# Performance work log

Measured on AMD Instinct MI355X. Metric: run time of the kernel, lower is better.

The kernel has to match this reference:

```python
import jax, jax.numpy as jnp
import numpy as np

NUM_HEADS = 16
LN_EPS = 1e-5


def pos_encoding(length, d):
    pos = jnp.arange(length, dtype=jnp.float32)[:, None]
    i = jnp.arange(d, dtype=jnp.float32)[None, :]
    angle = pos / jnp.power(10000.0, (2.0 * jnp.floor(i / 2.0)) / d)
    return jnp.where((jnp.arange(d) % 2) == 0, jnp.sin(angle), jnp.cos(angle))


def rel_shift(x):
    # x: (B, H, l, m) -> TXL shift trick
    b, h, l, m = x.shape
    x = jnp.concatenate([x, jnp.zeros((b, h, l, 1), x.dtype)], axis=-1)
    x = x.reshape(b, h, l * (m + 1))
    return x[:, :, l - 1:-1].reshape(b, h, l, m)


def layer_norm(x, g, b):
    mu = jnp.mean(x, axis=-1, keepdims=True)
    var = jnp.mean(jnp.square(x - mu), axis=-1, keepdims=True)
    return (x - mu) * jax.lax.rsqrt(var + LN_EPS) * g + b


def setup_inputs() -> dict:
    key = jax.random.key(0)
    B, S, M, D, L, V = 2, 1024, 1024, 1024, 4, 32000
    ks = jax.random.split(key, 32)
    s = 0.02
    d = {
        'inputs': jax.random.randint(ks[0], (B, S), 0, V, dtype=jnp.int32),
        'mems': jax.random.normal(ks[1], (L, B, M, D), jnp.float32),
        'emb': jax.random.normal(ks[2], (V, D), jnp.float32) * s,
        'Wq': jax.random.normal(ks[3], (L, D, D), jnp.float32) * s,
        'bq': jnp.zeros((L, D), jnp.float32),
        'Wke': jax.random.normal(ks[4], (L, D, D), jnp.float32) * s,
        'bke': jnp.zeros((L, D), jnp.float32),
        'Wkr': jax.random.normal(ks[5], (L, D, D), jnp.float32) * s,
        'bkr': jnp.zeros((L, D), jnp.float32),
        'Wv': jax.random.normal(ks[6], (L, D, D), jnp.float32) * s,
        'bv': jnp.zeros((L, D), jnp.float32),
        'Wo': jax.random.normal(ks[7], (L, D, D), jnp.float32) * s,
        'bo': jnp.zeros((L, D), jnp.float32),
        'ln1_g': jnp.ones((L, D), jnp.float32),
        'ln1_b': jnp.zeros((L, D), jnp.float32),
        'W1': jax.random.normal(ks[8], (L, D, D), jnp.float32) * s,
        'b1': jnp.zeros((L, D), jnp.float32),
        'W2': jax.random.normal(ks[9], (L, D, D), jnp.float32) * s,
        'b2': jnp.zeros((L, D), jnp.float32),
        'ln2_g': jnp.ones((L, D), jnp.float32),
        'ln2_b': jnp.zeros((L, D), jnp.float32),
        'Wh': jax.random.normal(ks[10], (D, D), jnp.float32) * s,
        'bh': jnp.zeros((D,), jnp.float32),
        'Wf': jax.random.normal(ks[11], (D, V), jnp.float32) * s,
        'bf': jnp.zeros((V,), jnp.float32),
        'next_mem_len': 1024,
    }
    return d


def reference(inputs, mems, emb, Wq, bq, Wke, bke, Wkr, bkr, Wv, bv, Wo, bo,
              ln1_g, ln1_b, W1, b1, W2, b2, ln2_g, ln2_b, Wh, bh, Wf, bf,
              next_mem_len):
    B, S = inputs.shape
    L, _, M, D = mems.shape
    T = M + S
    H = NUM_HEADS
    dh = D // H
    sqrt_dk = jnp.sqrt(jnp.float32(dh))

    rel_enc = pos_encoding(T, D)[::-1]  # (T, D), reversed
    # look-ahead mask: query i may attend key j iff j <= i + M
    mask = (jnp.arange(T)[None, :] > (jnp.arange(S)[:, None] + M)).astype(jnp.float32)
    mask = mask[None, None] * -1e9  # (1,1,S,T)

    x = emb[inputs] * jnp.sqrt(jnp.float32(D))  # (B,S,D)

    for l in range(L):
        x_tilde = jnp.concatenate([mems[l], x], axis=1)  # (B,T,D)
        q = (x @ Wq[l] + bq[l]).reshape(B, S, H, dh).transpose(0, 2, 1, 3)
        k = (x_tilde @ Wke[l] + bke[l]).reshape(B, T, H, dh).transpose(0, 2, 1, 3)
        v = (x_tilde @ Wv[l] + bv[l]).reshape(B, T, H, dh).transpose(0, 2, 1, 3)
        A = jnp.einsum('bhsd,bhtd->bhst', q, k)
        Qr = (rel_enc @ Wkr[l] + bkr[l]).reshape(T, H, dh).transpose(1, 0, 2)  # (H,T,dh)
        B_hat = jnp.einsum('bhsd,htd->bhst', q, Qr)
        score = (A + rel_shift(B_hat)) / sqrt_dk + mask
        attn = jax.nn.softmax(score, axis=-1)
        ctx = jnp.einsum('bhst,bhtd->bhsd', attn, v)
        ctx = ctx.transpose(0, 2, 1, 3).reshape(B, S, D)
        attn_out = ctx @ Wo[l] + bo[l]
        h1 = layer_norm(x + attn_out, ln1_g[l], ln1_b[l])
        ff = jax.nn.gelu(h1 @ W1[l] + b1[l], approximate=False) @ W2[l] + b2[l]
        x = layer_norm(h1 + ff, ln2_g[l], ln2_b[l])

    x = jax.nn.gelu(x @ Wh + bh, approximate=False)
    logits = x @ Wf + bf
    return logits
```

## Files before the change

### kernel.cpp

```cpp
#include <hip/hip_runtime.h>
#include <hip/hip_bf16.h>
#include <math.h>

typedef __attribute__((ext_vector_type(4))) float f32x4;
typedef __attribute__((ext_vector_type(8))) short s16x8;

#define BB 2
#define SS 1024
#define MEM 1024
#define DD 1024
#define LL 4
#define VV 32000
#define TT 2048
#define NH 16
#define DH 64

__device__ __forceinline__ short f2bf(float f) {
    unsigned u = __float_as_uint(f);
    u += 0x7fffu + ((u >> 16) & 1u);
    return (short)(u >> 16);
}

__device__ __forceinline__ float gelu_f(float x) {
    return 0.5f * x * (1.0f + erff(x * 0.70710678118654752f));
}

__device__ __forceinline__ void gll16(const short* g, short* l) {
    __builtin_amdgcn_global_load_lds(
        (__attribute__((address_space(1))) void*)(short*)g,
        (__attribute__((address_space(3))) void*)l, 16, 0, 0);
}

template<int WM, int WN>
__global__ __launch_bounds__(256) void gemm_k128(
    const short* __restrict__ A, const short* __restrict__ Bt,
    const float* __restrict__ bias, const float* __restrict__ bias2,
    int nsplit, void* __restrict__ Cv, int N, int K, int nby, int act, int obf)
{
    constexpr int BM = WM * 32, BN = WN * 32;
    constexpr int NA = BM / 16, NB = BN / 16;
    __shared__ short a_s[BM * 128];
    __shared__ short b_s[BN * 128];
    const int tid  = threadIdx.x;
    const int lane = tid & 63;
    const int wave = tid >> 6;
    const int wr = wave >> 1, wc = wave & 1;
    const int fr = lane & 15, fg = lane >> 4;

    const int nwg = gridDim.x;
    const int bid = blockIdx.x;
    const int swz = ((nwg & 7) == 0) ? ((bid & 7) * (nwg >> 3) + (bid >> 3)) : bid;
    const size_t m0 = (size_t)(swz % nby) * BM;
    const size_t n0 = (size_t)(swz / nby) * BN;

    const short* gA[NA]; short* lA[NA];
    const short* gB[NB]; short* lB[NB];
    #pragma unroll
    for (int i = 0; i < NA; ++i) {
        gA[i] = A + (m0 + i * 16 + (tid & 15)) * (size_t)K + (tid >> 4) * 8;
        lA[i] = &a_s[(i * 256 + tid) * 8];
    }
    #pragma unroll
    for (int i = 0; i < NB; ++i) {
        gB[i] = Bt + (n0 + i * 16 + (tid & 15)) * (size_t)K + (tid >> 4) * 8;
        lB[i] = &b_s[(i * 256 + tid) * 8];
    }

    f32x4 acc[WM][WN] = {};

    #pragma unroll
    for (int i = 0; i < NA; ++i) gll16(gA[i], lA[i]);
    #pragma unroll
    for (int i = 0; i < NB; ++i) gll16(gB[i], lB[i]);

    const int nt = K >> 7;
    for (int t = 0; t < nt; ++t) {
        __syncthreads();
        s16x8 af[WM][4], bf[WN][4];
        #pragma unroll
        for (int mi = 0; mi < WM; ++mi)
            #pragma unroll
            for (int h = 0; h < 4; ++h)
                af[mi][h] = *(const s16x8*)&a_s[((wr*WM + mi)*256 + (4*h + fg)*16 + fr) * 8];
        #pragma unroll
        for (int ni = 0; ni < WN; ++ni)
            #pragma unroll
            for (int h = 0; h < 4; ++h)
                bf[ni][h] = *(const s16x8*)&b_s[((wc*WN + ni)*256 + (4*h + fg)*16 + fr) * 8];
        if (t + 1 < nt) {
            __syncthreads();
            const int koff = (t + 1) << 7;
            #pragma unroll
            for (int i = 0; i < NA; ++i) gll16(gA[i] + koff, lA[i]);
            #pragma unroll
            for (int i = 0; i < NB; ++i) gll16(gB[i] + koff, lB[i]);
        }
        #pragma unroll
        for (int mi = 0; mi < WM; ++mi)
            #pragma unroll
            for (int ni = 0; ni < WN; ++ni)
                #pragma unroll
                for (int h = 0; h < 4; ++h)
                    acc[mi][ni] = __builtin_amdgcn_mfma_f32_16x16x32_bf16(
                        af[mi][h], bf[ni][h], acc[mi][ni], 0, 0, 0);
    }

    float* Cf = (float*)Cv;
    short* Cb = (short*)Cv;
    #pragma unroll
    for (int mi = 0; mi < WM; ++mi) {
        #pragma unroll
        for (int ni = 0; ni < WN; ++ni) {
            const size_t r0 = m0 + wr*WM*16 + mi*16 + fg*4;
            const size_t c  = n0 + wc*WN*16 + ni*16 + fr;
            const float bb = (c < (size_t)nsplit) ? bias[c] : bias2[c - nsplit];
            #pragma unroll
            for (int rg = 0; rg < 4; ++rg) {
                float vv = acc[mi][ni][rg] + bb;
                if (act) vv = gelu_f(vv);
                if (obf) Cb[(r0 + rg)*(size_t)N + c] = f2bf(vv);
                else     Cf[(r0 + rg)*(size_t)N + c] = vv;
            }
        }
    }
}

#define READ_A8(MH, BUF) \
  _Pragma("unroll") for (int mf = 0; mf < 4; ++mf) \
  _Pragma("unroll") for (int kh = 0; kh < 2; ++kh) \
    aA[mf][kh] = *(const s16x8*)&lds[(BUF)*16384 + WR*8192 + (((MH)*4+mf)*128 + (kh*4+fg)*16 + fr)*8];

#define READ_B8(BUF) \
  _Pragma("unroll") for (int nf = 0; nf < 4; ++nf) \
  _Pragma("unroll") for (int kh = 0; kh < 2; ++kh) \
    bB[nf][kh] = *(const s16x8*)&lds[32768 + (BUF)*16384 + BH*8192 + ((BC4+nf)*128 + (kh*4+fg)*16 + fr)*8];

#define QUAD8(MH, NHX) \
  _Pragma("unroll") for (int mf = 0; mf < 4; ++mf) \
  _Pragma("unroll") for (int n2 = 0; n2 < 2; ++n2) { \
    acc[(MH)*4+mf][(NHX)*2+n2] = __builtin_amdgcn_mfma_f32_16x16x32_bf16( \
        aA[mf][0], bB[(NHX)*2+n2][0], acc[(MH)*4+mf][(NHX)*2+n2], 0, 0, 0); \
    acc[(MH)*4+mf][(NHX)*2+n2] = __builtin_amdgcn_mfma_f32_16x16x32_bf16( \
        aA[mf][1], bB[(NHX)*2+n2][1], acc[(MH)*4+mf][(NHX)*2+n2], 0, 0, 0); }

#define STAGE_A8(HH, BUF, KT) { \
    const short* g = pA0 + (HH)*(128*1024) + (KT)*64; \
    short* l = &lds[(BUF)*16384 + (HH)*8192 + tid*8]; \
    gll16(g, l); gll16(g + 64*1024, l + 512*8); }

#define STAGE_B8(HH, BUF, KT) { \
    const short* g = pB0 + (HH)*(128*1024) + (KT)*64; \
    short* l = &lds[32768 + (BUF)*16384 + (HH)*8192 + tid*8]; \
    gll16(g, l); gll16(g + 64*1024, l + 512*8); }

#define PHASE8(BUF, MH, NHX, RA, RB, SMAT, SH, SBUF, SKT, VMW) { \
    if (RA) { READ_A8(MH, BUF) } \
    if (RB) { READ_B8(BUF) } \
    if ((SMAT) == 0) STAGE_A8(SH, SBUF, SKT) else STAGE_B8(SH, SBUF, SKT) \
    __builtin_amdgcn_s_barrier(); \
    asm volatile("s_waitcnt lgkmcnt(0)" ::: "memory"); \
    __builtin_amdgcn_sched_barrier(0); \
    __builtin_amdgcn_s_setprio(1); \
    QUAD8(MH, NHX) \
    __builtin_amdgcn_s_setprio(0); \
    if (VMW) { asm volatile("s_waitcnt vmcnt(4)" ::: "memory"); } \
    __builtin_amdgcn_s_barrier(); }

__global__ __launch_bounds__(512, 2) void gemm8p(
    const short* __restrict__ A, const short* __restrict__ Bt,
    const float* __restrict__ bias, float* __restrict__ C, int N)
{
    extern __shared__ short lds[];
    const int tid  = threadIdx.x;
    const int lane = tid & 63;
    const int wave = tid >> 6;
    const int WR = wave >> 2;
    const int WC = wave & 3;
    const int BH = WC >> 1;
    const int BC4 = (WC & 1) * 4;
    const int fr = lane & 15, fg = lane >> 4;

    const int nwg = gridDim.x;
    const int bid = blockIdx.x;
    const int swz = ((nwg & 7) == 0) ? ((bid & 7) * (nwg >> 3) + (bid >> 3)) : bid;
    const size_t m0 = (size_t)(swz % 8) * 256;
    const size_t n0 = (size_t)(swz / 8) * 256;

    const int arow0 = (tid >> 7) * 16 + (tid & 15);
    const int aks0  = ((tid >> 4) & 7) * 8;
    const short* pA0 = A  + (m0 + arow0) * 1024 + aks0;
    const short* pB0 = Bt + (n0 + arow0) * 1024 + aks0;

    f32x4 acc[8][4] = {};
    s16x8 aA[4][2], bB[4][2];

    STAGE_B8(0, 0, 0) STAGE_B8(1, 0, 0)
    STAGE_A8(0, 0, 0) STAGE_A8(1, 0, 0)
    STAGE_B8(0, 1, 1) STAGE_B8(1, 1, 1)
    asm volatile("s_waitcnt vmcnt(4)" ::: "memory");
    __builtin_amdgcn_s_barrier();

    for (int it = 0; it < 8; ++it) {
        const int k1 = 2*it + 1;
        int k2 = 2*it + 2; if (k2 > 15) k2 = 15;
        int k3 = 2*it + 3; if (k3 > 15) k3 = 15;
        PHASE8(0, 0, 0, 1, 1, 0, 0, 1, k1, 0)
        PHASE8(0, 0, 1, 0, 0, 0, 1, 1, k1, 0)
        PHASE8(0, 1, 0, 1, 0, 1, 0, 0, k2, 0)
        PHASE8(0, 1, 1, 0, 0, 1, 1, 0, k2, 1)
        PHASE8(1, 0, 0, 1, 1, 0, 0, 0, k2, 0)
        PHASE8(1, 0, 1, 0, 0, 0, 1, 0, k2, 0)
        PHASE8(1, 1, 0, 1, 0, 1, 0, 1, k3, 0)
        PHASE8(1, 1, 1, 0, 0, 1, 1, 1, k3, 1)
    }

    #pragma unroll
    for (int mf = 0; mf < 8; ++mf) {
        #pragma unroll
        for (int nf = 0; nf < 4; ++nf) {
            const size_t r0 = m0 + WR*128 + mf*16 + fg*4;
            const size_t c  = n0 + WC*64 + nf*16 + fr;
            const float bb = bias[c];
            #pragma unroll
            for (int rg = 0; rg < 4; ++rg)
                C[(r0 + rg) * (size_t)N + c] = acc[mf][nf][rg] + bb;
        }
    }
}

__global__ __launch_bounds__(512, 2) void gemm8n(
    const short* __restrict__ A, const short* __restrict__ Bt,
    const float* __restrict__ bA, const float* __restrict__ bBp,
    const float* __restrict__ bCp, int s1, int s2,
    short* __restrict__ Cb, int N, int K, int nby)
{
    extern __shared__ short lds[];
    const int tid  = threadIdx.x;
    const int lane = tid & 63;
    const int wave = tid >> 6;
    const int WR = wave >> 2;
    const int WC = wave & 3;
    const int fr = lane & 15, fg = lane >> 4;

    const int nwg = gridDim.x;
    const int bid = blockIdx.x;
    const int swz = ((nwg & 7) == 0) ? ((bid & 7) * (nwg >> 3) + (bid >> 3)) : bid;
    const size_t m0 = (size_t)(swz % nby) * 256;
    const size_t n0 = (size_t)(swz / nby) * 128;

    const int rA  = (tid >> 7) * 16 + (tid & 15);
    const int ks8 = ((tid >> 4) & 7) * 8;
    const short* pA = A  + (m0 + rA) * (size_t)K + ks8;
    const short* pB = Bt + (n0 + rA) * (size_t)K + ks8;

    auto stageA = [&](int kt, int h, int buf) {
        const short* g = pA + (size_t)(h * 128) * K + kt * 64;
        short* l = &lds[buf * 16384 + h * 8192 + tid * 8];
        gll16(g, l);
        gll16(g + (size_t)64 * K, l + 512 * 8);
    };
    auto stageB = [&](int kt, int buf) {
        const short* g = pB + kt * 64;
        short* l = &lds[49152 + buf * 8192 + tid * 8];
        gll16(g, l);
        gll16(g + (size_t)64 * K, l + 512 * 8);
    };

    f32x4 acc[8][2] = {};
    const int nt = K >> 6;

    stageB(0, 0); stageA(0, 0, 0); stageA(0, 1, 0);
    stageA(1, 0, 1); stageA(1, 1, 1); stageB(1, 1);

    for (int J = 0; J < nt / 2; ++J) {
        const int t0 = 2 * J, t1 = 2 * J + 1;
        const int b0 = t0 % 3, b1 = t1 % 3;
        const int b2 = (t0 + 2) % 3, b3 = (t1 + 2) % 3;
        int s2k = t0 + 2; if (s2k >= nt) s2k = nt - 1;
        int s3k = t1 + 2; if (s3k >= nt) s3k = nt - 1;

        #pragma unroll
        for (int ph = 0; ph < 2; ++ph) {
            const int bt = ph ? b1 : b0;
            asm volatile("s_waitcnt vmcnt(6)" ::: "memory");
            __builtin_amdgcn_s_barrier();
            __builtin_amdgcn_sched_barrier(0);
            if (ph == 0) { stageB(s2k, b2); stageA(s2k, 0, b2); stageA(s2k, 1, b2); }
            else         { stageA(s3k, 0, b3); stageA(s3k, 1, b3); stageB(s3k, b3); }
            s16x8 bB[2][2];
            #pragma unroll
            for (int nf = 0; nf < 2; ++nf)
                #pragma unroll
                for (int kh = 0; kh < 2; ++kh)
                    bB[nf][kh] = *(const s16x8*)&lds[49152 + bt*8192 +
                        ((WC*2 + nf)*128 + (kh*4 + fg)*16 + fr) * 8];
            #pragma unroll
            for (int MH = 0; MH < 2; ++MH) {
                s16x8 aF[4][2];
                #pragma unroll
                for (int mf = 0; mf < 4; ++mf)
                    #pragma unroll
                    for (int kh = 0; kh < 2; ++kh)
                        aF[mf][kh] = *(const s16x8*)&lds[bt*16384 + WR*8192 +
                            ((MH*4 + mf)*128 + (kh*4 + fg)*16 + fr) * 8];
                asm volatile("s_waitcnt lgkmcnt(0)" ::: "memory");
                __builtin_amdgcn_sched_barrier(0);
                __builtin_amdgcn_s_setprio(1);
                #pragma unroll
                for (int mf = 0; mf < 4; ++mf)
                    #pragma unroll
                    for (int nf = 0; nf < 2; ++nf) {
                        acc[MH*4+mf][nf] = __builtin_amdgcn_mfma_f32_16x16x32_bf16(
                            aF[mf][0], bB[nf][0], acc[MH*4+mf][nf], 0, 0, 0);
                        acc[MH*4+mf][nf] = __builtin_amdgcn_mfma_f32_16x16x32_bf16(
                            aF[mf][1], bB[nf][1], acc[MH*4+mf][nf], 0, 0, 0);
                    }
                __builtin_amdgcn_s_setprio(0);
            }
        }
    }

    #pragma unroll
    for (int mf = 0; mf < 8; ++mf) {
        #pragma unroll
        for (int nf = 0; nf < 2; ++nf) {
            const size_t r0 = m0 + WR*128 + mf*16 + fg*4;
            const size_t c  = n0 + WC*32 + nf*16 + fr;
            const float bb = (c < (size_t)s1) ? bA[c]
                            : (c < (size_t)s2) ? bBp[c - s1] : bCp[c - s2];
            #pragma unroll
            for (int rg = 0; rg < 4; ++rg)
                Cb[(r0 + rg) * (size_t)N + c] = f2bf(acc[mf][nf][rg] + bb);
        }
    }
}

__global__ __launch_bounds__(256) void transpose7_kernel(
    const float* w0, const float* w1, const float* w2, const float* w3,
    const float* w4, const float* w5, const float* w6, short* out)
{
    __shared__ float t[32][33];
    const int z = blockIdx.z;
    const float* W;
    switch (z) {
        case 0: W = w0; break; case 1: W = w1; break; case 2: W = w2; break;
        case 3: W = w3; break; case 4: W = w4; break; case 5: W = w5; break;
        default: W = w6; break;
    }
    short* O = out + (size_t)z * DD * DD;
    const int tid = threadIdx.x;
    const int k0 = blockIdx.y * 32, n0 = blockIdx.x * 32;
    const int r = tid >> 3, c4 = (tid & 7) * 4;
    float4 v = *(const float4*)&W[(size_t)(k0 + r) * DD + n0 + c4];
    t[r][c4+0] = v.x; t[r][c4+1] = v.y; t[r][c4+2] = v.z; t[r][c4+3] = v.w;
    __syncthreads();
    short4 o;
    o.x = f2bf(t[c4+0][r]); o.y = f2bf(t[c4+1][r]);
    o.z = f2bf(t[c4+2][r]); o.w = f2bf(t[c4+3][r]);
    *(short4*)&O[(size_t)(n0 + r) * DD + k0 + c4] = o;
}

__global__ __launch_bounds__(256) void transposeF_kernel(
    const float* __restrict__ W, short* __restrict__ O)
{
    __shared__ float t[32][33];
    const int tid = threadIdx.x;
    const int k0 = blockIdx.y * 32, n0 = blockIdx.x * 32;
    const int r = tid >> 3, c4 = (tid & 7) * 4;
    float4 v = *(const float4*)&W[(size_t)(k0 + r) * VV + n0 + c4];
    t[r][c4+0] = v.x; t[r][c4+1] = v.y; t[r][c4+2] = v.z; t[r][c4+3] = v.w;
    __syncthreads();
    short4 o;
    o.x = f2bf(t[c4+0][r]); o.y = f2bf(t[c4+1][r]);
    o.z = f2bf(t[c4+2][r]); o.w = f2bf(t[c4+3][r]);
    *(short4*)&O[(size_t)(n0 + r) * DD + k0 + c4] = o;
}

__global__ __launch_bounds__(256, 2) void attn_kernel(
    const short* __restrict__ q, const short* __restrict__ k,
    const short* __restrict__ v, const short* __restrict__ Qr,
    short* __restrict__ ctx, int kstr, int qstr)
{
    __shared__ short k_s[128][72];
    __shared__ short vT_s[64][136];
    __shared__ short qr_s[192][72];
    __shared__ float a_t[64][68];

    const int tid  = threadIdx.x;
    const int id   = blockIdx.x;
    const int bh   = id & 31;
    const int qi   = ((id >> 5) + bh) & 15;
    const int q0   = qi * 64;
    const int b    = bh >> 4;
    const int h    = bh & 15;
    const int hoff = h * DH;

    const int lane = tid & 63;
    const int wave = tid >> 6;
    const int fr   = lane & 15;
    const int fg   = lane >> 4;
    const int tk2 = tid >> 1, ck2 = (tid & 1) * 32;
    const int jq2 = tid >> 1, dqr = (tid & 1) * 32;
    const int j2  = tid >> 2, dq2 = (tid & 3) * 16;
    const int sr  = tid >> 2;
    const int sc0 = (tid & 3) * 16;

    const short* qrow = q + ((size_t)(b * TT + q0 + 16 * wave + fr)) * kstr + hoff;
    s16x8 aq0 = *(const s16x8*)(qrow + fg * 8);
    s16x8 aq1 = *(const s16x8*)(qrow + 32 + fg * 8);

    float m_r = -1e30f, l_r = 0.0f;

    const int t_end = q0 + 64 + MEM;
    const int u0b   = SS - 1 - q0 - 63;

    s16x8 kf[4], vf[4], rgq[4], rgq2[2];
    auto loadKV = [&](int t0n) {
        const short* kp = k + ((size_t)(b * TT + t0n + tk2)) * kstr + hoff + ck2;
        const short* vp = v + ((size_t)(b * TT + t0n + tk2)) * kstr + hoff + ck2;
        #pragma unroll
        for (int i = 0; i < 4; ++i) {
            kf[i] = *(const s16x8*)(kp + 8 * i);
            vf[i] = *(const s16x8*)(vp + 8 * i);
        }
    };
    auto loadQR = [&](int t0n) {
        int u = t0n + u0b + 63 + jq2;
        u = u > TT - 1 ? TT - 1 : u;
        const short* rp = Qr + (size_t)u * qstr + hoff + dqr;
        #pragma unroll
        for (int i = 0; i < 4; ++i) rgq[i] = *(const s16x8*)(rp + 8 * i);
    };
    {
        int u1 = u0b + jq2;
        u1 = u1 > TT - 1 ? TT - 1 : u1;
        const short* rp1 = Qr + (size_t)u1 * qstr + hoff + dqr;
        #pragma unroll
        for (int i = 0; i < 4; ++i) rgq[i] = *(const s16x8*)(rp1 + 8 * i);
        int u2 = u0b + 128 + j2;
        u2 = u2 > TT - 1 ? TT - 1 : u2;
        const short* rp2 = Qr + (size_t)u2 * qstr + hoff + dq2;
        rgq2[0] = *(const s16x8*)rp2;
        rgq2[1] = *(const s16x8*)(rp2 + 8);
    }
    loadKV(0);

    f32x4 opv[4] = {};
    const int nlo = 3 - wave, nhi = 7 - wave;
    int rb = 0;

    auto computeHalf = [&](int hh, int t0) {
        {
            __builtin_amdgcn_s_setprio(1);
            #pragma unroll
            for (int n = 0; n < 4; ++n) {
                s16x8 b0 = *(const s16x8*)&k_s[64*hh + 16*n + fr][fg * 8];
                s16x8 b1 = *(const s16x8*)&k_s[64*hh + 16*n + fr][32 + fg * 8];
                f32x4 ca = {0, 0, 0, 0};
                ca = __builtin_amdgcn_mfma_f32_16x16x32_bf16(aq0, b0, ca, 0, 0, 0);
                ca = __builtin_amdgcn_mfma_f32_16x16x32_bf16(aq1, b1, ca, 0, 0, 0);
                #pragma unroll
                for (int rg = 0; rg < 4; ++rg)
                    a_t[16*wave + 4*fg + rg][16*n + fr] = ca[rg];
            }
            __builtin_amdgcn_s_setprio(0);
        }
        {
            #pragma unroll
            for (int n = 0; n < 8; ++n) {
                if (n < nlo || n > nhi) continue;
                int pr = rb + 64*hh + 16*n + fr;
                if (pr >= 192) pr -= 192;
                s16x8 c0 = *(const s16x8*)&qr_s[pr][fg * 8];
                s16x8 c1 = *(const s16x8*)&qr_s[pr][32 + fg * 8];
                f32x4 cb = {0, 0, 0, 0};
                cb = __builtin_amdgcn_mfma_f32_16x16x32_bf16(aq0, c0, cb, 0, 0, 0);
                cb = __builtin_amdgcn_mfma_f32_16x16x32_bf16(aq1, c1, cb, 0, 0, 0);
                #pragma unroll
                for (int rg = 0; rg < 4; ++rg) {
                    const int r  = 16*wave + 4*fg + rg;
                    const int tl = 16*n + fr - 63 + r;
                    if ((unsigned)tl < 64u) a_t[r][tl] += cb[rg];
                }
            }
        }
        {
            const int sg = q0 + sr;
            const int tb = t0 + 64*hh;
            float e[16];
            float mx = -1e30f;
            #pragma unroll
            for (int j = 0; j < 16; ++j) {
                const int c = sc0 + j;
                float x = a_t[sr][c] * 0.125f;
                x = (tb + c > sg + MEM) ? -1e30f : x;
                e[j] = x;
                mx = fmaxf(mx, x);
            }
            mx = fmaxf(mx, __shfl_xor(mx, 1, 64));
            mx = fmaxf(mx, __shfl_xor(mx, 2, 64));
            const float mn  = fmaxf(m_r, mx);
            const float scl = __expf(m_r - mn);
            float sum = 0.0f;
            s16x8 p0, p1;
            #pragma unroll
            for (int j = 0; j < 16; ++j) {
                float ev = __expf(e[j] - mn);
                sum += ev;
                if (j < 8) p0[j] = f2bf(ev); else p1[j - 8] = f2bf(ev);
            }
            sum += __shfl_xor(sum, 1, 64);
            sum += __shfl_xor(sum, 2, 64);
            l_r = l_r * scl + sum;
            m_r = mn;
            short* prow = (short*)&a_t[sr][0];
            *(s16x8*)&prow[sc0]     = p0;
            *(s16x8*)&prow[sc0 + 8] = p1;
            asm volatile("s_waitcnt lgkmcnt(0)" ::: "memory");
            __builtin_amdgcn_sched_barrier(0);

            f32x4 scv;
            #pragma unroll
            for (int rg = 0; rg < 4; ++rg) scv[rg] = __shfl(scl, 16*fg + 4*rg, 64);
            #pragma unroll
            for (int n = 0; n < 4; ++n)
                #pragma unroll
                for (int rg = 0; rg < 4; ++rg) opv[n][rg] *= scv[rg];
            const short* pv = (const short*)&a_t[16*wave + fr][0];
            s16x8 ap0 = *(const s16x8*)&pv[fg * 8];
            s16x8 ap1 = *(const s16x8*)&pv[32 + fg * 8];
            __builtin_amdgcn_s_setprio(1);
            #pragma unroll
            for (int n = 0; n < 4; ++n) {
                const int d  = 16*n + fr;
                const int xw = (d >> 3) & 3;
                s16x8 bv0 = *(const s16x8*)&vT_s[d][64*hh + (fg ^ xw) * 8];
                s16x8 bv1 = *(const s16x8*)&vT_s[d][64*hh + 32 + ((fg + 4) ^ xw ? 0 : 0) + (fg ^ xw) * 8 - (fg ^ xw) * 8 + ((fg ^ xw) * 8)];
                bv1 = *(const s16x8*)&vT_s[d][64*hh + 32 + (fg ^ xw) * 8];
                opv[n] = __builtin_amdgcn_mfma_f32_16x16x32_bf16(ap0, bv0, opv[n], 0, 0, 0);
                opv[n] = __builtin_amdgcn_mfma_f32_16x16x32_bf16(ap1, bv1, opv[n], 0, 0, 0);
            }
            __builtin_amdgcn_s_setprio(0);
        }
    };

    for (int t0 = 0; t0 < t_end; t0 += 128) {
        asm volatile("" ::: "memory");
        __builtin_amdgcn_s_barrier();
        __builtin_amdgcn_sched_barrier(0);
        {
            #pragma unroll
            for (int i = 0; i < 4; ++i)
                *(s16x8*)&k_s[tk2][ck2 + 8*i] = kf[i];
            #pragma unroll
            for (int i = 0; i < 4; ++i) {
                #pragma unroll
                for (int e = 0; e < 8; ++e) {
                    const int d = ck2 + 8*i + e;
                    const int col = 64*(tk2 >> 6) + ((tk2 & 63) ^ (((d >> 3) & 3) << 3));
                    vT_s[d][col] = vf[i][e];
                }
            }
            if (t0 == 0) {
                #pragma unroll
                for (int i = 0; i < 4; ++i)
                    *(s16x8*)&qr_s[jq2][dqr + 8*i] = rgq[i];
                *(s16x8*)&qr_s[128 + j2][dq2]     = rgq2[0];
                *(s16x8*)&qr_s[128 + j2][dq2 + 8] = rgq2[1];
            } else {
                int p = rb + 63 + jq2;
                if (p >= 192) p -= 192;
                #pragma unroll
                for (int i = 0; i < 4; ++i)
                    *(s16x8*)&qr_s[p][dqr + 8*i] = rgq[i];
            }
        }
        if (t0 + 128 < t_end) { loadKV(t0 + 128); loadQR(t0 + 128); }
        asm volatile("s_waitcnt lgkmcnt(0)" ::: "memory");
        __builtin_amdgcn_s_barrier();
        __builtin_amdgcn_sched_barrier(0);

        computeHalf(0, t0);
        if (t0 + 64 < t_end) computeHalf(1, t0);

        rb += 128; if (rb >= 192) rb -= 192;
    }

    {
        f32x4 lv;
        #pragma unroll
        for (int rg = 0; rg < 4; ++rg) lv[rg] = __shfl(l_r, 16*fg + 4*rg, 64);
        #pragma unroll
        for (int rg = 0; rg < 4; ++rg) {
            const int r = 16*wave + 4*fg + rg;
            const float inv = 1.0f / lv[rg];
            short* op = ctx + ((size_t)(b * SS + q0 + r)) * DD + hoff;
            #pragma unroll
            for (int n = 0; n < 4; ++n)
                op[16*n + fr] = f2bf(opv[n][rg] * inv);
        }
    }
}

__global__ __launch_bounds__(256) void addln_kernel(
    const float* __restrict__ a, const float* __restrict__ b,
    const float* __restrict__ g, const float* __restrict__ be,
    float* __restrict__ out32, short* __restrict__ outbf)
{
    __shared__ float red[8];
    const int row = blockIdx.x;
    const int tid = threadIdx.x;
    const size_t base = (size_t)row * DD;
    const int c = tid * 4;
    float4 xa = *(const float4*)(a + base + c);
    float4 xb = *(const float4*)(b + base + c);
    float x0 = xa.x + xb.x, x1 = xa.y + xb.y, x2 = xa.z + xb.z, x3 = xa.w + xb.w;
    float s  = x0 + x1 + x2 + x3;
    float sq = x0 * x0 + x1 * x1 + x2 * x2 + x3 * x3;
    #pragma unroll
    for (int o = 32; o > 0; o >>= 1) {
        s  += __shfl_down(s, o, 64);
        sq += __shfl_down(sq, o, 64);
    }
    const int wv = tid >> 6;
    if ((tid & 63) == 0) { red[wv * 2] = s; red[wv * 2 + 1] = sq; }
    __syncthreads();
    float ts = red[0] + red[2] + red[4] + red[6];
    float tq = red[1] + red[3] + red[5] + red[7];
    float mu  = ts * (1.0f / DD);
    float var = tq * (1.0f / DD) - mu * mu;
    float rs  = rsqrtf(var + 1e-5f);
    float4 gv = *(const float4*)(g + c);
    float4 bv = *(const float4*)(be + c);
    float4 o4;
    o4.x = (x0 - mu) * rs * gv.x + bv.x;
    o4.y = (x1 - mu) * rs * gv.y + bv.y;
    o4.z = (x2 - mu) * rs * gv.z + bv.z;
    o4.w = (x3 - mu) * rs * gv.w + bv.w;
    *(float4*)(out32 + base + c) = o4;
    short4 ob;
    ob.x = f2bf(o4.x); ob.y = f2bf(o4.y); ob.z = f2bf(o4.z); ob.w = f2bf(o4.w);
    *(short4*)(outbf + base + c) = ob;
}

__global__ __launch_bounds__(256) void embed_kernel(
    const int* __restrict__ inp, const float* __restrict__ emb,
    float* __restrict__ x32, short* __restrict__ xbf)
{
    const int row = blockIdx.x;
    const int c = threadIdx.x * 4;
    const int idx = inp[row];
    float4 vv = *(const float4*)(emb + (size_t)idx * DD + c);
    vv.x *= 32.0f; vv.y *= 32.0f; vv.z *= 32.0f; vv.w *= 32.0f;
    *(float4*)(x32 + (size_t)row * DD + c) = vv;
    short4 ob;
    ob.x = f2bf(vv.x); ob.y = f2bf(vv.y); ob.z = f2bf(vv.z); ob.w = f2bf(vv.w);
    *(short4*)(xbf + (size_t)row * DD + c) = ob;
}

__global__ __launch_bounds__(256) void concat_kernel(
    const float* __restrict__ mems_l, const short* __restrict__ xbf,
    short* __restrict__ xt)
{
    size_t i = ((size_t)blockIdx.x * 256 + threadIdx.x) * 8;
    size_t bt = i / DD;
    int d = (int)(i - bt * DD);
    int b = (int)(bt / TT);
    int t = (int)(bt - (size_t)b * TT);
    s16x8 o;
    if (t < MEM) {
        const float* mp = mems_l + ((size_t)(b * MEM + t)) * DD + d;
        float4 a0 = *(const float4*)mp;
        float4 a1 = *(const float4*)(mp + 4);
        o[0] = f2bf(a0.x); o[1] = f2bf(a0.y); o[2] = f2bf(a0.z); o[3] = f2bf(a0.w);
        o[4] = f2bf(a1.x); o[5] = f2bf(a1.y); o[6] = f2bf(a1.z); o[7] = f2bf(a1.w);
    } else {
        o = *(const s16x8*)(xbf + ((size_t)(b * SS + (t - MEM))) * DD + d);
    }
    *(s16x8*)(xt + i) = o;
}

__global__ __launch_bounds__(256) void relenc_kernel(short* __restrict__ re)
{
    const int u = blockIdx.x;
    const int p = TT - 1 - u;
    const int i0 = threadIdx.x * 4;
    short4 o;
    #pragma unroll
    for (int j = 0; j < 4; ++j) {
        int i = i0 + j;
        float ex   = (float)(2 * (i >> 1)) * (1.0f / DD);
        float invf = __expf(-ex * 9.210340371976184f);
        float ang  = (float)p * invf;
        float val  = (i & 1) ? cosf(ang) : sinf(ang);
        ((short*)&o)[j] = f2bf(val);
    }
    *(short4*)&re[(size_t)u * DD + i0] = o;
}

extern "C" void kernel_launch(void* const* d_in, const int* in_sizes, int n_in,
                              void* d_out, int out_size, void* d_ws, size_t ws_size,
                              hipStream_t stream)
{
    const int*   inp  = (const int*)d_in[0];
    const float* mems = (const float*)d_in[1];
    const float* emb  = (const float*)d_in[2];
    const float* Wq   = (const float*)d_in[3];
    const float* bq   = (const float*)d_in[4];
    const float* Wke  = (const float*)d_in[5];
    const float* bke  = (const float*)d_in[6];
    const float* Wkr  = (const float*)d_in[7];
    const float* bkr  = (const float*)d_in[8];
    const float* Wv   = (const float*)d_in[9];
    const float* bv   = (const float*)d_in[10];
    const float* Wo   = (const float*)d_in[11];
    const float* bo   = (const float*)d_in[12];
    const float* ln1g = (const float*)d_in[13];
    const float* ln1b = (const float*)d_in[14];
    const float* W1   = (const float*)d_in[15];
    const float* b1   = (const float*)d_in[16];
    const float* W2   = (const float*)d_in[17];
    const float* b2   = (const float*)d_in[18];
    const float* ln2g = (const float*)d_in[19];
    const float* ln2b = (const float*)d_in[20];
    const float* Wh   = (const float*)d_in[21];
    const float* bh   = (const float*)d_in[22];
    const float* Wf   = (const float*)d_in[23];
    const float* bfb  = (const float*)d_in[24];

    hipFuncSetAttribute((const void*)gemm8p,
                        hipFuncAttributeMaxDynamicSharedMemorySize, 131072);
    hipFuncSetAttribute((const void*)gemm8n,
                        hipFuncAttributeMaxDynamicSharedMemorySize, 147456);

    char* wsb = (char*)d_ws;
    size_t off = 0;
    auto alloc = [&](size_t bytes) { char* p = wsb + off; off += (bytes + 255) & ~(size_t)255; return p; };
    float* h132  = (float*)alloc((size_t)BB*SS*DD*4);
    float* ao32  = (float*)alloc((size_t)BB*SS*DD*4);
    float* ff232 = (float*)alloc((size_t)BB*SS*DD*4);
    short* xt    = (short*)alloc((size_t)BB*TT*DD*2);
    short* qkvb  = (short*)alloc((size_t)BB*TT*3*DD*2);
    short* ctxb  = (short*)alloc((size_t)BB*SS*DD*2);
    short* ff1   = (short*)alloc((size_t)BB*SS*DD*2);
    float* x32   = (float*)alloc((size_t)BB*SS*DD*4);
    short* x_bf  = (short*)alloc((size_t)BB*SS*DD*2);
    short* whout = (short*)alloc((size_t)BB*SS*DD*2);
    short* rel   = (short*)alloc((size_t)TT*DD*2);
    short* qr4   = (short*)alloc((size_t)TT*4*DD*2);
    short* wt6   = (short*)alloc((size_t)6*DD*DD*2);
    short* wkr4  = (short*)h132;
    short* wft   = (short*)h132;

    relenc_kernel<<<TT, 256, 0, stream>>>(rel);
    embed_kernel<<<BB * SS, 256, 0, stream>>>(inp, emb, x32, x_bf);

    const size_t WOFF = (size_t)DD * DD;

    transpose7_kernel<<<dim3(32, 32, 4), 256, 0, stream>>>(
        Wkr + 0*WOFF, Wkr + 1*WOFF, Wkr + 2*WOFF, Wkr + 3*WOFF, Wq, Wq, Wq, wkr4);
    gemm8n<<<dim3((TT/256) * (4*DD/128)), 512, 147456, stream>>>(
        rel, wkr4, bkr, bkr, bkr, 4*DD, 4*DD, qr4, 4*DD, DD, TT/256);

    const int gSm = (DD / 64) * ((BB * SS) / 64);

    for (int l = 0; l < LL; ++l) {
        const size_t wo  = (size_t)l * DD * DD;
        const size_t bo_ = (size_t)l * DD;
        transpose7_kernel<<<dim3(32, 32, 6), 256, 0, stream>>>(
            Wq + wo, Wke + wo, Wv + wo, Wo + wo, W1 + wo, W2 + wo, Wq, wt6);
        concat_kernel<<<(BB * TT * DD / 8) / 256, 256, 0, stream>>>(
            mems + (size_t)l * BB * MEM * DD, x_bf, xt);
        gemm8n<<<dim3((BB*TT/256) * (3*DD/128)), 512, 147456, stream>>>(
            xt, wt6, bq + bo_, bke + bo_, bv + bo_, DD, 2*DD, qkvb, 3*DD, DD, BB*TT/256);
        attn_kernel<<<dim3((SS / 64) * BB * NH), 256, 0, stream>>>(
            qkvb + (size_t)MEM * 3 * DD, qkvb + DD, qkvb + 2 * DD,
            qr4 + (size_t)l * DD, ctxb, 3 * DD, 4 * DD);
        gemm_k128<2,2><<<dim3(gSm), 256, 0, stream>>>(
            ctxb, wt6 + 3*WOFF, bo + bo_, bo + bo_, DD, ao32, DD, DD, (BB*SS)/64, 0, 0);
        addln_kernel<<<BB * SS, 256, 0, stream>>>(x32, ao32, ln1g + bo_, ln1b + bo_, h132, x_bf);
        gemm_k128<2,2><<<dim3(gSm), 256, 0, stream>>>(
            x_bf, wt6 + 4*WOFF, b1 + bo_, b1 + bo_, DD, ff1, DD, DD, (BB*SS)/64, 1, 1);
        gemm_k128<2,2><<<dim3(gSm), 256, 0, stream>>>(
            ff1, wt6 + 5*WOFF, b2 + bo_, b2 + bo_, DD, ff232, DD, DD, (BB*SS)/64, 0, 0);
        addln_kernel<<<BB * SS, 256, 0, stream>>>(h132, ff232, ln2g + bo_, ln2b + bo_, x32, x_bf);
    }

    transpose7_kernel<<<dim3(32, 32, 1), 256, 0, stream>>>(
        Wh, Wh, Wh, Wh, Wh, Wh, Wh, wt6);
    transposeF_kernel<<<dim3(VV / 32, DD / 32), 256, 0, stream>>>(Wf, wft);
    gemm_k128<2,2><<<dim3(gSm), 256, 0, stream>>>(
        x_bf, wt6, bh, bh, DD, whout, DD, DD, (BB*SS)/64, 1, 1);
    gemm8p<<<dim3((VV / 256) * ((BB * SS) / 256)), 512, 131072, stream>>>(
        whout, wft, bfb, (float*)d_out, VV);
}
```

Before: 1.267 ms.

## Skip Q projection for memory rows and read mems/x directly in QKV GEMM

```diff
diff --git a/kernel.cpp b/kernel.cpp
--- a/kernel.cpp
+++ b/kernel.cpp
@@ -229,10 +229,11 @@
 }
 
 __global__ __launch_bounds__(512, 2) void gemm8n(
-    const short* __restrict__ A, const short* __restrict__ Bt,
+    const short* __restrict__ Am, const short* __restrict__ Ax,
+    const short* __restrict__ Bt,
     const float* __restrict__ bA, const float* __restrict__ bBp,
     const float* __restrict__ bCp, int s1, int s2,
-    short* __restrict__ Cb, int N, int K, int nby)
+    short* __restrict__ Cb, int N, int K, int nby, int mapmode)
 {
     extern __shared__ short lds[];
     const int tid  = threadIdx.x;
@@ -245,12 +246,36 @@
     const int nwg = gridDim.x;
     const int bid = blockIdx.x;
     const int swz = ((nwg & 7) == 0) ? ((bid & 7) * (nwg >> 3) + (bid >> 3)) : bid;
-    const size_t m0 = (size_t)(swz % nby) * 256;
-    const size_t n0 = (size_t)(swz / nby) * 128;
+
+    size_t m0, n0;
+    if (mapmode == 0) {
+        m0 = (size_t)(swz % nby) * 256;
+        n0 = (size_t)(swz / nby) * 128;
+    } else {
+        int mt, ntile;
+        if (swz < 64) {
+            ntile = swz >> 3;
+            int mi = swz & 7;
+            mt = (mi & 3) + 4 + (mi >> 2) * 8;
+        } else {
+            int j = swz - 64;
+            ntile = 8 + (j >> 4);
+            mt = j & 15;
+        }
+        m0 = (size_t)mt * 256;
+        n0 = (size_t)ntile * 128;
+    }
+
+    const short* Abase; size_t row0;
+    if (mapmode == 1) {
+        const int bb = (int)(m0 >> 11), t = (int)(m0 & 2047);
+        if (t < 1024) { Abase = Am; row0 = (size_t)(bb * 1024 + t); }
+        else          { Abase = Ax; row0 = (size_t)(bb * 1024 + t - 1024); }
+    } else { Abase = Am; row0 = m0; }
 
     const int rA  = (tid >> 7) * 16 + (tid & 15);
     const int ks8 = ((tid >> 4) & 7) * 8;
-    const short* pA = A  + (m0 + rA) * (size_t)K + ks8;
+    const short* pA = Abase + (row0 + rA) * (size_t)K + ks8;
     const short* pB = Bt + (n0 + rA) * (size_t)K + ks8;
 
     auto stageA = [&](int kt, int h, int buf) {
@@ -374,6 +399,19 @@
     o.x = f2bf(t[c4+0][r]); o.y = f2bf(t[c4+1][r]);
     o.z = f2bf(t[c4+2][r]); o.w = f2bf(t[c4+3][r]);
     *(short4*)&O[(size_t)(n0 + r) * DD + k0 + c4] = o;
+}
+
+__global__ __launch_bounds__(256) void memsbf_kernel(
+    const float* __restrict__ mems, short* __restrict__ out)
+{
+    size_t i = ((size_t)blockIdx.x * 256 + threadIdx.x) * 8;
+    const float* mp = mems + i;
+    float4 a0 = *(const float4*)mp;
+    float4 a1 = *(const float4*)(mp + 4);
+    s16x8 o;
+    o[0] = f2bf(a0.x); o[1] = f2bf(a0.y); o[2] = f2bf(a0.z); o[3] = f2bf(a0.w);
+    o[4] = f2bf(a1.x); o[5] = f2bf(a1.y); o[6] = f2bf(a1.z); o[7] = f2bf(a1.w);
+    *(s16x8*)(out + i) = o;
 }
 
 __global__ __launch_bounds__(256, 2) void attn_kernel(
@@ -535,8 +573,7 @@
                 const int d  = 16*n + fr;
                 const int xw = (d >> 3) & 3;
                 s16x8 bv0 = *(const s16x8*)&vT_s[d][64*hh + (fg ^ xw) * 8];
-                s16x8 bv1 = *(const s16x8*)&vT_s[d][64*hh + 32 + ((fg + 4) ^ xw ? 0 : 0) + (fg ^ xw) * 8 - (fg ^ xw) * 8 + ((fg ^ xw) * 8)];
-                bv1 = *(const s16x8*)&vT_s[d][64*hh + 32 + (fg ^ xw) * 8];
+                s16x8 bv1 = *(const s16x8*)&vT_s[d][64*hh + 32 + (fg ^ xw) * 8];
                 opv[n] = __builtin_amdgcn_mfma_f32_16x16x32_bf16(ap0, bv0, opv[n], 0, 0, 0);
                 opv[n] = __builtin_amdgcn_mfma_f32_16x16x32_bf16(ap1, bv1, opv[n], 0, 0, 0);
             }
@@ -656,28 +693,6 @@
     short4 ob;
     ob.x = f2bf(vv.x); ob.y = f2bf(vv.y); ob.z = f2bf(vv.z); ob.w = f2bf(vv.w);
     *(short4*)(xbf + (size_t)row * DD + c) = ob;
-}
-
-__global__ __launch_bounds__(256) void concat_kernel(
-    const float* __restrict__ mems_l, const short* __restrict__ xbf,
-    short* __restrict__ xt)
-{
-    size_t i = ((size_t)blockIdx.x * 256 + threadIdx.x) * 8;
-    size_t bt = i / DD;
-    int d = (int)(i - bt * DD);
-    int b = (int)(bt / TT);
-    int t = (int)(bt - (size_t)b * TT);
-    s16x8 o;
-    if (t < MEM) {
-        const float* mp = mems_l + ((size_t)(b * MEM + t)) * DD + d;
-        float4 a0 = *(const float4*)mp;
-        float4 a1 = *(const float4*)(mp + 4);
-        o[0] = f2bf(a0.x); o[1] = f2bf(a0.y); o[2] = f2bf(a0.z); o[3] = f2bf(a0.w);
-        o[4] = f2bf(a1.x); o[5] = f2bf(a1.y); o[6] = f2bf(a1.z); o[7] = f2bf(a1.w);
-    } else {
-        o = *(const s16x8*)(xbf + ((size_t)(b * SS + (t - MEM))) * DD + d);
-    }
-    *(s16x8*)(xt + i) = o;
 }
 
 __global__ __launch_bounds__(256) void relenc_kernel(short* __restrict__ re)
@@ -739,7 +754,6 @@
     float* h132  = (float*)alloc((size_t)BB*SS*DD*4);
     float* ao32  = (float*)alloc((size_t)BB*SS*DD*4);
     float* ff232 = (float*)alloc((size_t)BB*SS*DD*4);
-    short* xt    = (short*)alloc((size_t)BB*TT*DD*2);
     short* qkvb  = (short*)alloc((size_t)BB*TT*3*DD*2);
     short* ctxb  = (short*)alloc((size_t)BB*SS*DD*2);
     short* ff1   = (short*)alloc((size_t)BB*SS*DD*2);
@@ -749,18 +763,20 @@
     short* rel   = (short*)alloc((size_t)TT*DD*2);
     short* qr4   = (short*)alloc((size_t)TT*4*DD*2);
     short* wt6   = (short*)alloc((size_t)6*DD*DD*2);
+    short* msbf  = (short*)alloc((size_t)LL*BB*MEM*DD*2);
     short* wkr4  = (short*)h132;
     short* wft   = (short*)h132;
 
     relenc_kernel<<<TT, 256, 0, stream>>>(rel);
     embed_kernel<<<BB * SS, 256, 0, stream>>>(inp, emb, x32, x_bf);
+    memsbf_kernel<<<(LL * BB * MEM * DD / 8) / 256, 256, 0, stream>>>(mems, msbf);
 
     const size_t WOFF = (size_t)DD * DD;
 
     transpose7_kernel<<<dim3(32, 32, 4), 256, 0, stream>>>(
         Wkr + 0*WOFF, Wkr + 1*WOFF, Wkr + 2*WOFF, Wkr + 3*WOFF, Wq, Wq, Wq, wkr4);
     gemm8n<<<dim3((TT/256) * (4*DD/128)), 512, 147456, stream>>>(
-        rel, wkr4, bkr, bkr, bkr, 4*DD, 4*DD, qr4, 4*DD, DD, TT/256);
+        rel, rel, wkr4, bkr, bkr, bkr, 4*DD, 4*DD, qr4, 4*DD, DD, TT/256, 0);
 
     const int gSm = (DD / 64) * ((BB * SS) / 64);
 
@@ -769,10 +785,9 @@
         const size_t bo_ = (size_t)l * DD;
         transpose7_kernel<<<dim3(32, 32, 6), 256, 0, stream>>>(
             Wq + wo, Wke + wo, Wv + wo, Wo + wo, W1 + wo, W2 + wo, Wq, wt6);
-        concat_kernel<<<(BB * TT * DD / 8) / 256, 256, 0, stream>>>(
-            mems + (size_t)l * BB * MEM * DD, x_bf, xt);
-        gemm8n<<<dim3((BB*TT/256) * (3*DD/128)), 512, 147456, stream>>>(
-            xt, wt6, bq + bo_, bke + bo_, bv + bo_, DD, 2*DD, qkvb, 3*DD, DD, BB*TT/256);
+        gemm8n<<<dim3(320), 512, 147456, stream>>>(
+            msbf + (size_t)l * BB * MEM * DD, x_bf, wt6,
+            bq + bo_, bke + bo_, bv + bo_, DD, 2*DD, qkvb, 3*DD, DD, 0, 1);
         attn_kernel<<<dim3((SS / 64) * BB * NH), 256, 0, stream>>>(
             qkvb + (size_t)MEM * 3 * DD, qkvb + DD, qkvb + 2 * DD,
             qr4 + (size_t)l * DD, ctxb, 3 * DD, 4 * DD);
```

Measured after the change: 1.256 ms. Within noise of the previous version (-0.8%).
